# Kernel optimization log

Hardware: AMD Instinct MI355X
Metric: run time of the kernel (lower is better)

Reference implementation:

```python
import jax, jax.numpy as jnp
import numpy as np

B, S, E, H = 2, 2048, 1024, 16
D = E // H


def setup_inputs() -> dict:
    key = jax.random.key(0)
    ks = jax.random.split(key, 8)
    q = jax.random.normal(ks[0], (B, S, E), dtype=jnp.float32)
    k = jax.random.normal(ks[1], (B, S, E), dtype=jnp.float32)
    v = jax.random.normal(ks[2], (B, S, E), dtype=jnp.float32)
    mask = jax.random.randint(ks[3], (B, 1, 1, S), 0, 2, dtype=jnp.int32)
    sc = 1.0 / np.sqrt(E)
    W_qkv = jax.random.normal(ks[4], (3 * E, E), dtype=jnp.float32) * sc
    b_qkv = jnp.zeros((3 * E,), dtype=jnp.float32)
    W_out = jax.random.normal(ks[5], (E, E), dtype=jnp.float32) * sc
    b_out = jnp.zeros((E,), dtype=jnp.float32)
    return {"q": q, "k": k, "v": v, "mask": mask,
            "W_qkv": W_qkv, "b_qkv": b_qkv, "W_out": W_out, "b_out": b_out}


def reference(q, k, v, mask, W_qkv, b_qkv, W_out, b_out):
    # Fused qkv linear: q takes the Q-slice, k the K-slice, v the V-slice.
    qp = (q @ W_qkv[:E].T + b_qkv[:E]).reshape(B, S, H, D)
    kp = (k @ W_qkv[E:2 * E].T + b_qkv[E:2 * E]).reshape(B, S, H, D)
    vp = (v @ W_qkv[2 * E:].T + b_qkv[2 * E:]).reshape(B, S, H, D)
    # (B,H,S,S) scores -- NOTE: original module does NOT scale by sqrt(d)
    energy = jnp.einsum('nqhd,nkhd->nhqk', qp, kp)
    energy = jnp.where(mask == 0, jnp.float32(-1e20), energy)
    attention = jax.nn.softmax(energy, axis=-1)
    out = jnp.einsum('nhql,nlhd->nqhd', attention, vp).reshape(B, S, E)
    return out @ W_out.T + b_out
```

## Files before the change

kernel.cpp:

```cpp
#include <hip/hip_runtime.h>
#include <stdint.h>

constexpr int B_ = 2, S_ = 2048, E_ = 1024, H_ = 16, D_ = 64;
constexpr int M_ = B_ * S_;
constexpr size_t ME_ = (size_t)M_ * E_;

typedef unsigned short u16;
typedef __attribute__((ext_vector_type(8))) short short8;
typedef __attribute__((ext_vector_type(4))) float f32x4;

__device__ __forceinline__ float bf2f(u16 u) {
  union { uint32_t i; float f; } v; v.i = ((uint32_t)u) << 16; return v.f;
}
__device__ __forceinline__ u16 f2bf(float f) {
  uint32_t u = __float_as_uint(f);
  return (u16)((u + 0x7FFFu + ((u >> 16) & 1u)) >> 16);
}
__device__ __forceinline__ void tsplit(float x, u16& hi, u16& lo) {
  const uint32_t u = __float_as_uint(x);
  hi = (u16)(u >> 16);
  const float hif = __uint_as_float(u & 0xFFFF0000u);
  lo = (u16)(__float_as_uint(x - hif) >> 16);
}

__global__ __launch_bounds__(256) void split_f32_kernel(
    const float* __restrict__ src, u16* __restrict__ hi, u16* __restrict__ lo, int n4)
{
  const int i = blockIdx.x * 256 + threadIdx.x;
  if (i >= n4) return;
  const float4 x = ((const float4*)src)[i];
  ushort4 h, l;
  tsplit(x.x, h.x, l.x); tsplit(x.y, h.y, l.y);
  tsplit(x.z, h.z, l.z); tsplit(x.w, h.w, l.w);
  ((ushort4*)hi)[i] = h;
  ((ushort4*)lo)[i] = l;
}

__global__ __launch_bounds__(256) void mask_scan_kernel(
    const int* __restrict__ mask, int* __restrict__ cpos, int* __restrict__ nk)
{
  __shared__ int tmp[256];
  __shared__ int coff;
  const int b = blockIdx.x, t = threadIdx.x;
  if (t == 0) coff = 0;
  __syncthreads();
  for (int c = 0; c < S_; c += 256) {
    const int m = (mask[b * S_ + c + t] != 0) ? 1 : 0;
    int x = m;
    tmp[t] = x;
    __syncthreads();
#pragma unroll
    for (int off = 1; off < 256; off <<= 1) {
      const int v = (t >= off) ? tmp[t - off] : 0;
      __syncthreads();
      x += v;
      tmp[t] = x;
      __syncthreads();
    }
    const int base = coff;
    cpos[b * S_ + c + t] = base + x - m;
    __syncthreads();
    if (t == 255) coff = base + x;
    __syncthreads();
  }
  if (t == 0) nk[b] = coff;
}

__global__ __launch_bounds__(256) void gemm_qkv_kernel(
    const float* __restrict__ q, const float* __restrict__ k, const float* __restrict__ v,
    const u16* __restrict__ WHi, const u16* __restrict__ WLo,
    const float* __restrict__ bias,
    const int* __restrict__ Msk, const int* __restrict__ Cpos,
    u16* __restrict__ QpHi, u16* __restrict__ QpLo,
    u16* __restrict__ KpHi, u16* __restrict__ KpLo,
    u16* __restrict__ Vp)
{
  __shared__ __align__(16) short smem[15360];
  short* Ah = smem;
  short* Al = smem + 5120;
  short* Bh = smem + 10240;
  short* Bl = smem + 12800;

  const int t = threadIdx.x;
  const int m0 = blockIdx.x * 128;
  const int n0g = blockIdx.y * 64;
  const int proj = n0g >> 10;
  const int nloc = n0g & (E_ - 1);
  const float* A = (proj == 0) ? q : (proj == 1) ? k : v;
  const bool split = (proj < 2);

  const int w = t >> 6, lane = t & 63;
  const int g = lane >> 4, lc = lane & 15;
  const int wm = w & 1, wn = w >> 1;
  const int sra = t >> 1, sca = (t & 1) * 16;
  const int srb = t >> 2, scb = (t & 3) * 8;

  const float* Abp = A + (size_t)(m0 + sra) * E_ + sca;
  const u16* Bhb = WHi + (size_t)(n0g + srb) * E_ + scb;
  const u16* Blb = WLo + (size_t)(n0g + srb) * E_ + scb;

  f32x4 acc[4][2];
#pragma unroll
  for (int i = 0; i < 4; ++i)
#pragma unroll
    for (int j = 0; j < 2; ++j) acc[i][j] = (f32x4){0.f, 0.f, 0.f, 0.f};

  float4 ar[4]; short8 br, cr;
#pragma unroll
  for (int i = 0; i < 4; ++i) ar[i] = *(const float4*)(Abp + 4 * i);
  br = *(const short8*)(Bhb);
  if (split) cr = *(const short8*)(Blb);

  for (int k0 = 0; k0 < E_; k0 += 32) {
    __syncthreads();
#pragma unroll
    for (int i = 0; i < 4; ++i) {
      ushort4 h, l;
      tsplit(ar[i].x, h.x, l.x); tsplit(ar[i].y, h.y, l.y);
      tsplit(ar[i].z, h.z, l.z); tsplit(ar[i].w, h.w, l.w);
      *(ushort4*)&Ah[sra * 40 + sca + 4 * i] = h;
      if (split) *(ushort4*)&Al[sra * 40 + sca + 4 * i] = l;
    }
    *(short8*)&Bh[srb * 40 + scb] = br;
    if (split) *(short8*)&Bl[srb * 40 + scb] = cr;
    __syncthreads();
    if (k0 + 32 < E_) {
#pragma unroll
      for (int i = 0; i < 4; ++i) ar[i] = *(const float4*)(Abp + k0 + 32 + 4 * i);
      br = *(const short8*)(Bhb + k0 + 32);
      if (split) cr = *(const short8*)(Blb + k0 + 32);
    }

    short8 ah[4], al[4], bh[2], bl[2];
#pragma unroll
    for (int mt = 0; mt < 4; ++mt) {
      const int ro = (wm * 64 + mt * 16 + lc) * 40 + g * 8;
      ah[mt] = *(const short8*)&Ah[ro];
      if (split) al[mt] = *(const short8*)&Al[ro];
    }
#pragma unroll
    for (int nt = 0; nt < 2; ++nt) {
      const int ro = (wn * 32 + nt * 16 + lc) * 40 + g * 8;
      bh[nt] = *(const short8*)&Bh[ro];
      if (split) bl[nt] = *(const short8*)&Bl[ro];
    }
#pragma unroll
    for (int mt = 0; mt < 4; ++mt)
#pragma unroll
      for (int nt = 0; nt < 2; ++nt) {
        f32x4 a = acc[mt][nt];
        a = __builtin_amdgcn_mfma_f32_16x16x32_bf16(ah[mt], bh[nt], a, 0, 0, 0);
        if (split) {
          a = __builtin_amdgcn_mfma_f32_16x16x32_bf16(ah[mt], bl[nt], a, 0, 0, 0);
          a = __builtin_amdgcn_mfma_f32_16x16x32_bf16(al[mt], bh[nt], a, 0, 0, 0);
        }
        acc[mt][nt] = a;
      }
  }

  float bs[2];
#pragma unroll
  for (int nt = 0; nt < 2; ++nt) bs[nt] = bias[n0g + wn * 32 + nt * 16 + lc];

  if (proj < 2) {
    u16* Hi = (proj == 0) ? QpHi : KpHi;
    u16* Lo = (proj == 0) ? QpLo : KpLo;
    const int head = nloc >> 6;
    short* T = smem + w * 2560;
    const int mrow = m0 + wm * 64 + lane;
    const int bb = mrow >> 11, s = mrow & (S_ - 1);
    bool ok = true;
    int srow_out = s;
    if (proj == 1) {
      ok = (Msk[bb * S_ + s] != 0);
      srow_out = Cpos[bb * S_ + s];
    }
    const size_t rowb = (((size_t)(bb * H_ + head)) * S_ + srow_out) * D_ + wn * 32;
#pragma unroll
    for (int pass = 0; pass < 2; ++pass) {
      __syncthreads();
#pragma unroll
      for (int nt = 0; nt < 2; ++nt)
#pragma unroll
        for (int mt = 0; mt < 4; ++mt)
#pragma unroll
          for (int r = 0; r < 4; ++r) {
            const float val = acc[mt][nt][r] + bs[nt];
            const uint32_t u = __float_as_uint(val);
            u16 x;
            if (pass == 0) x = (u16)(u >> 16);
            else {
              const float hif = __uint_as_float(u & 0xFFFF0000u);
              x = (u16)(__float_as_uint(val - hif) >> 16);
            }
            T[(mt * 16 + g * 4 + r) * 40 + nt * 16 + lc] = (short)x;
          }
      __syncthreads();
      u16* dst = (pass == 0) ? Hi : Lo;
      if (ok) {
#pragma unroll
        for (int j = 0; j < 4; ++j)
          *(short8*)&dst[rowb + 8 * j] = *(const short8*)&T[lane * 40 + 8 * j];
      }
    }
  } else {
#pragma unroll
    for (int mt = 0; mt < 4; ++mt) {
      const int mrow = m0 + wm * 64 + mt * 16 + g * 4;
      const int bb = mrow >> 11, sbase = mrow & (S_ - 1);
      const int4 mk = *(const int4*)&Msk[bb * S_ + sbase];
      const int4 cp = *(const int4*)&Cpos[bb * S_ + sbase];
      const int mkA[4] = {mk.x, mk.y, mk.z, mk.w};
      const int cpA[4] = {cp.x, cp.y, cp.z, cp.w};
#pragma unroll
      for (int nt = 0; nt < 2; ++nt) {
        const int nE = nloc + wn * 32 + nt * 16 + lc;
        const int h = nE >> 6, d = nE & 63;
        const size_t rb = (((size_t)(bb * H_ + h)) * D_ + d) * S_;
#pragma unroll
        for (int r = 0; r < 4; ++r) {
          if (mkA[r]) Vp[rb + cpA[r]] = f2bf(acc[mt][nt][r] + bs[nt]);
        }
      }
    }
  }
}

__global__ __launch_bounds__(256, 4) void attn_mfma_kernel(
    const u16* __restrict__ QpHi, const u16* __restrict__ QpLo,
    const u16* __restrict__ KpHi, const u16* __restrict__ KpLo,
    const u16* __restrict__ Vp,
    const int* __restrict__ nkArr,
    u16* __restrict__ AOHi)
{
  __shared__ __align__(16) short sm[18432];
  short* Khi = sm;
  short* Klo = sm + 4608;
  short* Vt  = sm + 9216;
  short* Pb  = sm + 13824;

  const int t = threadIdx.x;
  const int w = t >> 6, lane = t & 63;
  const int g = lane >> 4, lc = lane & 15;
  const int bh = blockIdx.y;
  const int b = bh >> 4, hh = bh & 15;
  const int q0 = blockIdx.x * 64;
  const size_t hb = (size_t)bh * S_ * D_;
  const u16* QgH = QpHi + hb;
  const u16* QgL = QpLo + hb;
  const u16* KgH = KpHi + hb;
  const u16* KgL = KpLo + hb;
  const u16* Vg  = Vp + hb;
  short* Pw = Pb + w * 1152;

  const int nk = nkArr[b];
  const int kend = ((nk + 63) >> 6) << 6;

  short8 qh[2], ql[2];
  {
    const size_t base = (size_t)(q0 + 16 * w + lc) * D_ + 8 * g;
    qh[0] = *(const short8*)&QgH[base];
    qh[1] = *(const short8*)&QgH[base + 32];
    ql[0] = *(const short8*)&QgL[base];
    ql[1] = *(const short8*)&QgL[base + 32];
  }

  short8 ones8 = {0, 0, 0, 0, 0, 0, 0, 0};
  if (lc == 0) {
    const short o = (short)0x3F80;
    ones8 = (short8){o, o, o, o, o, o, o, o};
  }

  f32x4 O[4];
  f32x4 Ol = (f32x4){0.f, 0.f, 0.f, 0.f};
#pragma unroll
  for (int dt = 0; dt < 4; ++dt) O[dt] = (f32x4){0.f, 0.f, 0.f, 0.f};
  float mst[4] = {-INFINITY, -INFINITY, -INFINITY, -INFINITY};

  const int srow = t >> 2, sc16 = (t & 3) * 16;

  short8 kr[2], lr[2], vr[2];
  kr[0] = *(const short8*)&KgH[srow * D_ + sc16];
  kr[1] = *(const short8*)&KgH[srow * D_ + sc16 + 8];
  lr[0] = *(const short8*)&KgL[srow * D_ + sc16];
  lr[1] = *(const short8*)&KgL[srow * D_ + sc16 + 8];
  vr[0] = *(const short8*)&Vg[srow * S_ + sc16];
  vr[1] = *(const short8*)&Vg[srow * S_ + sc16 + 8];

  for (int kt = 0; kt < kend; kt += 64) {
    __syncthreads();
    *(short8*)&Khi[srow * 72 + sc16]     = kr[0];
    *(short8*)&Khi[srow * 72 + sc16 + 8] = kr[1];
    *(short8*)&Klo[srow * 72 + sc16]     = lr[0];
    *(short8*)&Klo[srow * 72 + sc16 + 8] = lr[1];
    *(short8*)&Vt[srow * 72 + sc16]      = vr[0];
    *(short8*)&Vt[srow * 72 + sc16 + 8]  = vr[1];
    __syncthreads();
    if (kt + 64 < kend) {
      const int kn = kt + 64;
      kr[0] = *(const short8*)&KgH[(kn + srow) * D_ + sc16];
      kr[1] = *(const short8*)&KgH[(kn + srow) * D_ + sc16 + 8];
      lr[0] = *(const short8*)&KgL[(kn + srow) * D_ + sc16];
      lr[1] = *(const short8*)&KgL[(kn + srow) * D_ + sc16 + 8];
      vr[0] = *(const short8*)&Vg[srow * S_ + kn + sc16];
      vr[1] = *(const short8*)&Vg[srow * S_ + kn + sc16 + 8];
    }

    f32x4 sc[4];
#pragma unroll
    for (int kt16 = 0; kt16 < 4; ++kt16) {
      const int ko = (16 * kt16 + lc) * 72 + 8 * g;
      const short8 kh0 = *(const short8*)&Khi[ko];
      const short8 kh1 = *(const short8*)&Khi[ko + 32];
      const short8 kl0 = *(const short8*)&Klo[ko];
      const short8 kl1 = *(const short8*)&Klo[ko + 32];
      f32x4 a = {0.f, 0.f, 0.f, 0.f};
      a = __builtin_amdgcn_mfma_f32_16x16x32_bf16(qh[0], kh0, a, 0, 0, 0);
      a = __builtin_amdgcn_mfma_f32_16x16x32_bf16(qh[1], kh1, a, 0, 0, 0);
      a = __builtin_amdgcn_mfma_f32_16x16x32_bf16(qh[0], kl0, a, 0, 0, 0);
      a = __builtin_amdgcn_mfma_f32_16x16x32_bf16(qh[1], kl1, a, 0, 0, 0);
      a = __builtin_amdgcn_mfma_f32_16x16x32_bf16(ql[0], kh0, a, 0, 0, 0);
      a = __builtin_amdgcn_mfma_f32_16x16x32_bf16(ql[1], kh1, a, 0, 0, 0);
      sc[kt16] = a;
    }

    if (kt + 64 > nk) {
#pragma unroll
      for (int kt16 = 0; kt16 < 4; ++kt16) {
        if (kt + 16 * kt16 + lc >= nk) {
          sc[kt16][0] = -1e20f; sc[kt16][1] = -1e20f;
          sc[kt16][2] = -1e20f; sc[kt16][3] = -1e20f;
        }
      }
    }

    float al[4];
#pragma unroll
    for (int r = 0; r < 4; ++r) {
      float vv = fmaxf(fmaxf(sc[0][r], sc[1][r]), fmaxf(sc[2][r], sc[3][r]));
      vv = fmaxf(vv, __shfl_xor(vv, 1));
      vv = fmaxf(vv, __shfl_xor(vv, 2));
      vv = fmaxf(vv, __shfl_xor(vv, 4));
      vv = fmaxf(vv, __shfl_xor(vv, 8));
      const float mn = fmaxf(mst[r], vv);
      al[r] = __expf(mst[r] - mn);
      mst[r] = mn;
    }
#pragma unroll
    for (int kt16 = 0; kt16 < 4; ++kt16) {
#pragma unroll
      for (int r = 0; r < 4; ++r)
        sc[kt16][r] = __expf(sc[kt16][r] - mst[r]);
    }
    const f32x4 alv = {al[0], al[1], al[2], al[3]};
    O[0] *= alv; O[1] *= alv; O[2] *= alv; O[3] *= alv;
    Ol *= alv;
#pragma unroll
    for (int kt16 = 0; kt16 < 4; ++kt16) {
#pragma unroll
      for (int r = 0; r < 4; ++r)
        Pw[(4 * g + r) * 72 + 16 * kt16 + lc] = (short)f2bf(sc[kt16][r]);
    }

    short8 pa[2];
    pa[0] = *(const short8*)&Pw[lc * 72 + 8 * g];
    pa[1] = *(const short8*)&Pw[lc * 72 + 32 + 8 * g];
    Ol = __builtin_amdgcn_mfma_f32_16x16x32_bf16(pa[0], ones8, Ol, 0, 0, 0);
    Ol = __builtin_amdgcn_mfma_f32_16x16x32_bf16(pa[1], ones8, Ol, 0, 0, 0);
#pragma unroll
    for (int dt = 0; dt < 4; ++dt) {
      const int vo = (16 * dt + lc) * 72 + 8 * g;
      const short8 vb0 = *(const short8*)&Vt[vo];
      const short8 vb1 = *(const short8*)&Vt[vo + 32];
      O[dt] = __builtin_amdgcn_mfma_f32_16x16x32_bf16(pa[0], vb0, O[dt], 0, 0, 0);
      O[dt] = __builtin_amdgcn_mfma_f32_16x16x32_bf16(pa[1], vb1, O[dt], 0, 0, 0);
    }
  }

#pragma unroll
  for (int r = 0; r < 4; ++r) {
    const float lv = __shfl(Ol[r], lane & 48);
    const float lir = 1.0f / lv;
    const int qrow = q0 + 16 * w + 4 * g + r;
    const size_t rowb = (size_t)(b * S_ + qrow) * E_ + hh * 64;
#pragma unroll
    for (int dt = 0; dt < 4; ++dt)
      AOHi[rowb + dt * 16 + lc] = f2bf(O[dt][r] * lir);
  }
}

__global__ __launch_bounds__(256) void gemm_out_kernel(
    const u16* __restrict__ AHi,
    const u16* __restrict__ WHi,
    const float* __restrict__ bias, float* __restrict__ out)
{
  __shared__ __align__(16) short Ah[128 * 40];
  __shared__ __align__(16) short Bh[128 * 40];

  const int t = threadIdx.x;
  const int m0 = blockIdx.x * 128;
  const int n0 = blockIdx.y * 128;
  const int w = t >> 6, lane = t & 63;
  const int g = lane >> 4, lc = lane & 15;
  const int wm = w & 1, wn = w >> 1;
  const int srow = t >> 1, sh = (t & 1) * 16;

  const u16* Ahb = AHi + (size_t)(m0 + srow) * E_ + sh;
  const u16* Bhb = WHi + (size_t)(n0 + srow) * E_ + sh;

  f32x4 acc[4][4];
#pragma unroll
  for (int i = 0; i < 4; ++i)
#pragma unroll
    for (int j = 0; j < 4; ++j) acc[i][j] = (f32x4){0.f, 0.f, 0.f, 0.f};

  short8 arr[2], brr[2];
  arr[0] = *(const short8*)(Ahb); arr[1] = *(const short8*)(Ahb + 8);
  brr[0] = *(const short8*)(Bhb); brr[1] = *(const short8*)(Bhb + 8);

  for (int k0 = 0; k0 < E_; k0 += 32) {
    __syncthreads();
    *(short8*)&Ah[srow * 40 + sh]     = arr[0];
    *(short8*)&Ah[srow * 40 + sh + 8] = arr[1];
    *(short8*)&Bh[srow * 40 + sh]     = brr[0];
    *(short8*)&Bh[srow * 40 + sh + 8] = brr[1];
    __syncthreads();
    if (k0 + 32 < E_) {
      arr[0] = *(const short8*)(Ahb + k0 + 32); arr[1] = *(const short8*)(Ahb + k0 + 40);
      brr[0] = *(const short8*)(Bhb + k0 + 32); brr[1] = *(const short8*)(Bhb + k0 + 40);
    }

    short8 ah[4], bh[4];
#pragma unroll
    for (int mt = 0; mt < 4; ++mt)
      ah[mt] = *(const short8*)&Ah[(wm * 64 + mt * 16 + lc) * 40 + g * 8];
#pragma unroll
    for (int nt = 0; nt < 4; ++nt)
      bh[nt] = *(const short8*)&Bh[(wn * 64 + nt * 16 + lc) * 40 + g * 8];
#pragma unroll
    for (int mt = 0; mt < 4; ++mt)
#pragma unroll
      for (int nt = 0; nt < 4; ++nt)
        acc[mt][nt] = __builtin_amdgcn_mfma_f32_16x16x32_bf16(ah[mt], bh[nt], acc[mt][nt], 0, 0, 0);
  }

  float bs[4];
#pragma unroll
  for (int nt = 0; nt < 4; ++nt) bs[nt] = bias[n0 + wn * 64 + nt * 16 + lc];
#pragma unroll
  for (int nt = 0; nt < 4; ++nt) {
    const int nc = n0 + wn * 64 + nt * 16 + lc;
#pragma unroll
    for (int mt = 0; mt < 4; ++mt) {
#pragma unroll
      for (int r = 0; r < 4; ++r) {
        const int mrow = m0 + wm * 64 + mt * 16 + g * 4 + r;
        out[(size_t)mrow * E_ + nc] = acc[mt][nt][r] + bs[nt];
      }
    }
  }
}

extern "C" void kernel_launch(void* const* d_in, const int* in_sizes, int n_in,
                              void* d_out, int out_size, void* d_ws, size_t ws_size,
                              hipStream_t stream) {
  const float* q    = (const float*)d_in[0];
  const float* k    = (const float*)d_in[1];
  const float* v    = (const float*)d_in[2];
  const int*   mask = (const int*)d_in[3];
  const float* Wqkv = (const float*)d_in[4];
  const float* bqkv = (const float*)d_in[5];
  const float* Wout = (const float*)d_in[6];
  const float* bout = (const float*)d_in[7];
  float* out = (float*)d_out;

  char* wsb = (char*)d_ws;
  u16* WqkvHi = (u16*)(wsb + 0);
  u16* WqkvLo = (u16*)(wsb + 6291456);
  u16* WoutHi = (u16*)(wsb + 12582912);
  int* Cpos   = (int*)(wsb + 14680064);
  int* Nk     = (int*)(wsb + 14680064 + 16384);
  u16* WoutLo = (u16*)(wsb + 14680064);
  u16* QpHi   = (u16*)(wsb + 16777216);
  u16* QpLo   = (u16*)(wsb + 25165824);
  u16* KpHi   = (u16*)(wsb + 33554432);
  u16* KpLo   = (u16*)(wsb + 41943040);
  u16* Vp     = (u16*)(wsb + 50331648);
  u16* AOHi   = (u16*)(wsb + 58720256);

  hipLaunchKernelGGL(split_f32_kernel, dim3(3072), dim3(256), 0, stream,
                     Wqkv, WqkvHi, WqkvLo, 786432);
  hipLaunchKernelGGL(split_f32_kernel, dim3(1024), dim3(256), 0, stream,
                     Wout, WoutHi, WoutLo, 262144);
  hipLaunchKernelGGL(mask_scan_kernel, dim3(B_), dim3(256), 0, stream,
                     mask, Cpos, Nk);
  hipMemsetAsync(Vp, 0, 8388608, stream);
  hipLaunchKernelGGL(gemm_qkv_kernel, dim3(M_ / 128, 48), dim3(256), 0, stream,
                     q, k, v, WqkvHi, WqkvLo, bqkv, mask, Cpos,
                     QpHi, QpLo, KpHi, KpLo, Vp);
  hipLaunchKernelGGL(attn_mfma_kernel, dim3(S_ / 64, B_ * H_), dim3(256), 0, stream,
                     QpHi, QpLo, KpHi, KpLo, Vp, Nk, AOHi);
  hipLaunchKernelGGL(gemm_out_kernel, dim3(M_ / 128, E_ / 128), dim3(256), 0, stream,
                     AOHi, WoutHi, bout, out);
}
```

Before: 294.4 us.

## Gather unmasked K/V rows before projection, double-buffer GEMM LDS, retile output GEMM

```diff
diff --git a/kernel.cpp b/kernel.cpp
--- a/kernel.cpp
+++ b/kernel.cpp
@@ -3,15 +3,11 @@
 
 constexpr int B_ = 2, S_ = 2048, E_ = 1024, H_ = 16, D_ = 64;
 constexpr int M_ = B_ * S_;
-constexpr size_t ME_ = (size_t)M_ * E_;
 
 typedef unsigned short u16;
 typedef __attribute__((ext_vector_type(8))) short short8;
 typedef __attribute__((ext_vector_type(4))) float f32x4;
 
-__device__ __forceinline__ float bf2f(u16 u) {
-  union { uint32_t i; float f; } v; v.i = ((uint32_t)u) << 16; return v.f;
-}
 __device__ __forceinline__ u16 f2bf(float f) {
   uint32_t u = __float_as_uint(f);
   return (u16)((u + 0x7FFFu + ((u >> 16) & 1u)) >> 16);
@@ -21,6 +17,13 @@
   hi = (u16)(u >> 16);
   const float hif = __uint_as_float(u & 0xFFFF0000u);
   lo = (u16)(__float_as_uint(x - hif) >> 16);
+}
+
+__device__ __forceinline__ void block_sync() {
+  asm volatile("" ::: "memory");
+  asm volatile("s_waitcnt lgkmcnt(0)" ::: "memory");
+  __builtin_amdgcn_s_barrier();
+  asm volatile("" ::: "memory");
 }
 
 __global__ __launch_bounds__(256) void split_f32_kernel(
@@ -37,11 +40,12 @@
 }
 
 __global__ __launch_bounds__(256) void mask_scan_kernel(
-    const int* __restrict__ mask, int* __restrict__ cpos, int* __restrict__ nk)
+    const int* __restrict__ mask, int* __restrict__ opos, int* __restrict__ nk)
 {
   __shared__ int tmp[256];
   __shared__ int coff;
   const int b = blockIdx.x, t = threadIdx.x;
+  for (int c = t; c < S_; c += 256) opos[b * S_ + c] = 0;
   if (t == 0) coff = 0;
   __syncthreads();
   for (int c = 0; c < S_; c += 256) {
@@ -58,7 +62,7 @@
       __syncthreads();
     }
     const int base = coff;
-    cpos[b * S_ + c + t] = base + x - m;
+    if (m) opos[b * S_ + base + x - 1] = c + t;
     __syncthreads();
     if (t == 255) coff = base + x;
     __syncthreads();
@@ -66,38 +70,45 @@
   if (t == 0) nk[b] = coff;
 }
 
-__global__ __launch_bounds__(256) void gemm_qkv_kernel(
+__global__ __launch_bounds__(256, 3) void gemm_qkv_kernel(
     const float* __restrict__ q, const float* __restrict__ k, const float* __restrict__ v,
     const u16* __restrict__ WHi, const u16* __restrict__ WLo,
     const float* __restrict__ bias,
-    const int* __restrict__ Msk, const int* __restrict__ Cpos,
+    const int* __restrict__ Opos, const int* __restrict__ NkArr,
     u16* __restrict__ QpHi, u16* __restrict__ QpLo,
     u16* __restrict__ KpHi, u16* __restrict__ KpLo,
     u16* __restrict__ Vp)
 {
-  __shared__ __align__(16) short smem[15360];
-  short* Ah = smem;
-  short* Al = smem + 5120;
-  short* Bh = smem + 10240;
-  short* Bl = smem + 12800;
+  __shared__ __align__(16) short smem[20480];
+  short* Ah0 = smem;
+  short* Al0 = smem + 5120;
+  short* Ah1 = smem + 10240;
+  short* Al1 = smem + 15360;
 
   const int t = threadIdx.x;
   const int m0 = blockIdx.x * 128;
   const int n0g = blockIdx.y * 64;
   const int proj = n0g >> 10;
   const int nloc = n0g & (E_ - 1);
+  const bool split = (proj < 2);
+  const int bb = m0 >> 11, mloc = m0 & (S_ - 1);
+  const int nkb = NkArr[bb];
+  if (proj != 0 && mloc >= nkb) return;
+
   const float* A = (proj == 0) ? q : (proj == 1) ? k : v;
-  const bool split = (proj < 2);
 
   const int w = t >> 6, lane = t & 63;
   const int g = lane >> 4, lc = lane & 15;
   const int wm = w & 1, wn = w >> 1;
   const int sra = t >> 1, sca = (t & 1) * 16;
-  const int srb = t >> 2, scb = (t & 3) * 8;
-
-  const float* Abp = A + (size_t)(m0 + sra) * E_ + sca;
-  const u16* Bhb = WHi + (size_t)(n0g + srb) * E_ + scb;
-  const u16* Blb = WLo + (size_t)(n0g + srb) * E_ + scb;
+
+  int arow;
+  if (proj == 0) arow = m0 + sra;
+  else arow = bb * S_ + (Opos[bb * S_ + mloc + sra] & (S_ - 1));
+  const float* Abp = A + (size_t)arow * E_ + sca;
+
+  const u16* BHrow = WHi + (size_t)(n0g + wn * 32 + lc) * E_ + 8 * g;
+  const u16* BLrow = WLo + (size_t)(n0g + wn * 32 + lc) * E_ + 8 * g;
 
   f32x4 acc[4][2];
 #pragma unroll
@@ -105,33 +116,29 @@
 #pragma unroll
     for (int j = 0; j < 2; ++j) acc[i][j] = (f32x4){0.f, 0.f, 0.f, 0.f};
 
-  float4 ar[4]; short8 br, cr;
-#pragma unroll
-  for (int i = 0; i < 4; ++i) ar[i] = *(const float4*)(Abp + 4 * i);
-  br = *(const short8*)(Bhb);
-  if (split) cr = *(const short8*)(Blb);
-
-  for (int k0 = 0; k0 < E_; k0 += 32) {
-    __syncthreads();
+  auto loadA = [&](float4* ar, int kk) {
+#pragma unroll
+    for (int i = 0; i < 4; ++i) ar[i] = *(const float4*)(Abp + kk + 4 * i);
+  };
+  auto writeA = [&](const float4* ar, short* Ah, short* Al) {
+    ushort hh[16], ll[16];
 #pragma unroll
     for (int i = 0; i < 4; ++i) {
-      ushort4 h, l;
-      tsplit(ar[i].x, h.x, l.x); tsplit(ar[i].y, h.y, l.y);
-      tsplit(ar[i].z, h.z, l.z); tsplit(ar[i].w, h.w, l.w);
-      *(ushort4*)&Ah[sra * 40 + sca + 4 * i] = h;
-      if (split) *(ushort4*)&Al[sra * 40 + sca + 4 * i] = l;
-    }
-    *(short8*)&Bh[srb * 40 + scb] = br;
-    if (split) *(short8*)&Bl[srb * 40 + scb] = cr;
-    __syncthreads();
-    if (k0 + 32 < E_) {
-#pragma unroll
-      for (int i = 0; i < 4; ++i) ar[i] = *(const float4*)(Abp + k0 + 32 + 4 * i);
-      br = *(const short8*)(Bhb + k0 + 32);
-      if (split) cr = *(const short8*)(Blb + k0 + 32);
-    }
-
-    short8 ah[4], al[4], bh[2], bl[2];
+      tsplit(ar[i].x, hh[4 * i + 0], ll[4 * i + 0]);
+      tsplit(ar[i].y, hh[4 * i + 1], ll[4 * i + 1]);
+      tsplit(ar[i].z, hh[4 * i + 2], ll[4 * i + 2]);
+      tsplit(ar[i].w, hh[4 * i + 3], ll[4 * i + 3]);
+    }
+    *(short8*)&Ah[sra * 40 + sca]     = *(const short8*)&hh[0];
+    *(short8*)&Ah[sra * 40 + sca + 8] = *(const short8*)&hh[8];
+    if (split) {
+      *(short8*)&Al[sra * 40 + sca]     = *(const short8*)&ll[0];
+      *(short8*)&Al[sra * 40 + sca + 8] = *(const short8*)&ll[8];
+    }
+  };
+  auto compute = [&](const short* Ah, const short* Al,
+                     short8 bh0, short8 bh1, short8 bl0, short8 bl1) {
+    short8 ah[4], al[4];
 #pragma unroll
     for (int mt = 0; mt < 4; ++mt) {
       const int ro = (wm * 64 + mt * 16 + lc) * 40 + g * 8;
@@ -139,23 +146,51 @@
       if (split) al[mt] = *(const short8*)&Al[ro];
     }
 #pragma unroll
-    for (int nt = 0; nt < 2; ++nt) {
-      const int ro = (wn * 32 + nt * 16 + lc) * 40 + g * 8;
-      bh[nt] = *(const short8*)&Bh[ro];
-      if (split) bl[nt] = *(const short8*)&Bl[ro];
-    }
-#pragma unroll
-    for (int mt = 0; mt < 4; ++mt)
-#pragma unroll
-      for (int nt = 0; nt < 2; ++nt) {
-        f32x4 a = acc[mt][nt];
-        a = __builtin_amdgcn_mfma_f32_16x16x32_bf16(ah[mt], bh[nt], a, 0, 0, 0);
-        if (split) {
-          a = __builtin_amdgcn_mfma_f32_16x16x32_bf16(ah[mt], bl[nt], a, 0, 0, 0);
-          a = __builtin_amdgcn_mfma_f32_16x16x32_bf16(al[mt], bh[nt], a, 0, 0, 0);
-        }
-        acc[mt][nt] = a;
+    for (int mt = 0; mt < 4; ++mt) {
+      f32x4 a0 = acc[mt][0], a1 = acc[mt][1];
+      a0 = __builtin_amdgcn_mfma_f32_16x16x32_bf16(ah[mt], bh0, a0, 0, 0, 0);
+      a1 = __builtin_amdgcn_mfma_f32_16x16x32_bf16(ah[mt], bh1, a1, 0, 0, 0);
+      if (split) {
+        a0 = __builtin_amdgcn_mfma_f32_16x16x32_bf16(ah[mt], bl0, a0, 0, 0, 0);
+        a0 = __builtin_amdgcn_mfma_f32_16x16x32_bf16(al[mt], bh0, a0, 0, 0, 0);
+        a1 = __builtin_amdgcn_mfma_f32_16x16x32_bf16(ah[mt], bl1, a1, 0, 0, 0);
+        a1 = __builtin_amdgcn_mfma_f32_16x16x32_bf16(al[mt], bh1, a1, 0, 0, 0);
       }
+      acc[mt][0] = a0; acc[mt][1] = a1;
+    }
+  };
+
+  float4 arA[4], arB[4];
+  short8 b0h0, b0h1, b1h0, b1h1;
+  short8 b0l0 = {}, b0l1 = {}, b1l0 = {}, b1l1 = {};
+  loadA(arA, 0);
+  b0h0 = *(const short8*)(BHrow);
+  b0h1 = *(const short8*)(BHrow + 16 * E_);
+  if (split) { b0l0 = *(const short8*)(BLrow); b0l1 = *(const short8*)(BLrow + 16 * E_); }
+
+  for (int k0 = 0; k0 < E_; k0 += 64) {
+    loadA(arB, k0 + 32);
+    writeA(arA, Ah0, Al0);
+    block_sync();
+    b1h0 = *(const short8*)(BHrow + k0 + 32);
+    b1h1 = *(const short8*)(BHrow + 16 * E_ + k0 + 32);
+    if (split) {
+      b1l0 = *(const short8*)(BLrow + k0 + 32);
+      b1l1 = *(const short8*)(BLrow + 16 * E_ + k0 + 32);
+    }
+    compute(Ah0, Al0, b0h0, b0h1, b0l0, b0l1);
+
+    const int kn = (k0 + 64 < E_) ? (k0 + 64) : 0;
+    loadA(arA, kn);
+    writeA(arB, Ah1, Al1);
+    block_sync();
+    b0h0 = *(const short8*)(BHrow + kn);
+    b0h1 = *(const short8*)(BHrow + 16 * E_ + kn);
+    if (split) {
+      b0l0 = *(const short8*)(BLrow + kn);
+      b0l1 = *(const short8*)(BLrow + 16 * E_ + kn);
+    }
+    compute(Ah1, Al1, b1h0, b1h1, b1l0, b1l1);
   }
 
   float bs[2];
@@ -167,15 +202,8 @@
     u16* Lo = (proj == 0) ? QpLo : KpLo;
     const int head = nloc >> 6;
     short* T = smem + w * 2560;
-    const int mrow = m0 + wm * 64 + lane;
-    const int bb = mrow >> 11, s = mrow & (S_ - 1);
-    bool ok = true;
-    int srow_out = s;
-    if (proj == 1) {
-      ok = (Msk[bb * S_ + s] != 0);
-      srow_out = Cpos[bb * S_ + s];
-    }
-    const size_t rowb = (((size_t)(bb * H_ + head)) * S_ + srow_out) * D_ + wn * 32;
+    const int s = (m0 + wm * 64 + lane) & (S_ - 1);
+    const size_t rowb = (((size_t)(bb * H_ + head)) * S_ + s) * D_ + wn * 32;
 #pragma unroll
     for (int pass = 0; pass < 2; ++pass) {
       __syncthreads();
@@ -197,21 +225,14 @@
           }
       __syncthreads();
       u16* dst = (pass == 0) ? Hi : Lo;
-      if (ok) {
-#pragma unroll
-        for (int j = 0; j < 4; ++j)
-          *(short8*)&dst[rowb + 8 * j] = *(const short8*)&T[lane * 40 + 8 * j];
-      }
+#pragma unroll
+      for (int j = 0; j < 4; ++j)
+        *(short8*)&dst[rowb + 8 * j] = *(const short8*)&T[lane * 40 + 8 * j];
     }
   } else {
 #pragma unroll
     for (int mt = 0; mt < 4; ++mt) {
-      const int mrow = m0 + wm * 64 + mt * 16 + g * 4;
-      const int bb = mrow >> 11, sbase = mrow & (S_ - 1);
-      const int4 mk = *(const int4*)&Msk[bb * S_ + sbase];
-      const int4 cp = *(const int4*)&Cpos[bb * S_ + sbase];
-      const int mkA[4] = {mk.x, mk.y, mk.z, mk.w};
-      const int cpA[4] = {cp.x, cp.y, cp.z, cp.w};
+      const int jb = mloc + wm * 64 + mt * 16 + g * 4;
 #pragma unroll
       for (int nt = 0; nt < 2; ++nt) {
         const int nE = nloc + wn * 32 + nt * 16 + lc;
@@ -219,7 +240,7 @@
         const size_t rb = (((size_t)(bb * H_ + h)) * D_ + d) * S_;
 #pragma unroll
         for (int r = 0; r < 4; ++r) {
-          if (mkA[r]) Vp[rb + cpA[r]] = f2bf(acc[mt][nt][r] + bs[nt]);
+          if (jb + r < nkb) Vp[rb + jb + r] = f2bf(acc[mt][nt][r] + bs[nt]);
         }
       }
     }
@@ -394,69 +415,66 @@
     const u16* __restrict__ WHi,
     const float* __restrict__ bias, float* __restrict__ out)
 {
-  __shared__ __align__(16) short Ah[128 * 40];
-  __shared__ __align__(16) short Bh[128 * 40];
+  __shared__ __align__(16) short smem[5120];
+  short* A0 = smem;
+  short* A1 = smem + 2560;
 
   const int t = threadIdx.x;
-  const int m0 = blockIdx.x * 128;
-  const int n0 = blockIdx.y * 128;
+  const int m0 = blockIdx.x * 64;
+  const int n0 = blockIdx.y * 64;
   const int w = t >> 6, lane = t & 63;
   const int g = lane >> 4, lc = lane & 15;
-  const int wm = w & 1, wn = w >> 1;
-  const int srow = t >> 1, sh = (t & 1) * 16;
-
-  const u16* Ahb = AHi + (size_t)(m0 + srow) * E_ + sh;
-  const u16* Bhb = WHi + (size_t)(n0 + srow) * E_ + sh;
-
-  f32x4 acc[4][4];
-#pragma unroll
-  for (int i = 0; i < 4; ++i)
-#pragma unroll
-    for (int j = 0; j < 4; ++j) acc[i][j] = (f32x4){0.f, 0.f, 0.f, 0.f};
-
-  short8 arr[2], brr[2];
-  arr[0] = *(const short8*)(Ahb); arr[1] = *(const short8*)(Ahb + 8);
-  brr[0] = *(const short8*)(Bhb); brr[1] = *(const short8*)(Bhb + 8);
-
-  for (int k0 = 0; k0 < E_; k0 += 32) {
-    __syncthreads();
-    *(short8*)&Ah[srow * 40 + sh]     = arr[0];
-    *(short8*)&Ah[srow * 40 + sh + 8] = arr[1];
-    *(short8*)&Bh[srow * 40 + sh]     = brr[0];
-    *(short8*)&Bh[srow * 40 + sh + 8] = brr[1];
-    __syncthreads();
-    if (k0 + 32 < E_) {
-      arr[0] = *(const short8*)(Ahb + k0 + 32); arr[1] = *(const short8*)(Ahb + k0 + 40);
-      brr[0] = *(const short8*)(Bhb + k0 + 32); brr[1] = *(const short8*)(Bhb + k0 + 40);
-    }
-
-    short8 ah[4], bh[4];
-#pragma unroll
-    for (int mt = 0; mt < 4; ++mt)
-      ah[mt] = *(const short8*)&Ah[(wm * 64 + mt * 16 + lc) * 40 + g * 8];
-#pragma unroll
-    for (int nt = 0; nt < 4; ++nt)
-      bh[nt] = *(const short8*)&Bh[(wn * 64 + nt * 16 + lc) * 40 + g * 8];
-#pragma unroll
-    for (int mt = 0; mt < 4; ++mt)
-#pragma unroll
-      for (int nt = 0; nt < 4; ++nt)
-        acc[mt][nt] = __builtin_amdgcn_mfma_f32_16x16x32_bf16(ah[mt], bh[nt], acc[mt][nt], 0, 0, 0);
-  }
-
-  float bs[4];
-#pragma unroll
-  for (int nt = 0; nt < 4; ++nt) bs[nt] = bias[n0 + wn * 64 + nt * 16 + lc];
-#pragma unroll
-  for (int nt = 0; nt < 4; ++nt) {
-    const int nc = n0 + wn * 64 + nt * 16 + lc;
-#pragma unroll
-    for (int mt = 0; mt < 4; ++mt) {
-#pragma unroll
-      for (int r = 0; r < 4; ++r) {
-        const int mrow = m0 + wm * 64 + mt * 16 + g * 4 + r;
-        out[(size_t)mrow * E_ + nc] = acc[mt][nt][r] + bs[nt];
-      }
+  const int srb = t >> 2, scb = (t & 3) * 8;
+
+  const u16* Abp = AHi + (size_t)(m0 + srb) * E_ + scb;
+  const u16* Brow = WHi + (size_t)(n0 + w * 16 + lc) * E_ + 8 * g;
+
+  f32x4 acc[4];
+#pragma unroll
+  for (int i = 0; i < 4; ++i) acc[i] = (f32x4){0.f, 0.f, 0.f, 0.f};
+
+  short8 aA, aB, b0, b1;
+  aA = *(const short8*)(Abp);
+  b0 = *(const short8*)(Brow);
+
+  for (int k0 = 0; k0 < E_; k0 += 64) {
+    aB = *(const short8*)(Abp + k0 + 32);
+    *(short8*)&A0[srb * 40 + scb] = aA;
+    block_sync();
+    b1 = *(const short8*)(Brow + k0 + 32);
+    {
+      short8 ah[4];
+#pragma unroll
+      for (int mt = 0; mt < 4; ++mt)
+        ah[mt] = *(const short8*)&A0[(mt * 16 + lc) * 40 + g * 8];
+#pragma unroll
+      for (int mt = 0; mt < 4; ++mt)
+        acc[mt] = __builtin_amdgcn_mfma_f32_16x16x32_bf16(ah[mt], b0, acc[mt], 0, 0, 0);
+    }
+    const int kn = (k0 + 64 < E_) ? (k0 + 64) : 0;
+    aA = *(const short8*)(Abp + kn);
+    *(short8*)&A1[srb * 40 + scb] = aB;
+    block_sync();
+    b0 = *(const short8*)(Brow + kn);
+    {
+      short8 ah[4];
+#pragma unroll
+      for (int mt = 0; mt < 4; ++mt)
+        ah[mt] = *(const short8*)&A1[(mt * 16 + lc) * 40 + g * 8];
+#pragma unroll
+      for (int mt = 0; mt < 4; ++mt)
+        acc[mt] = __builtin_amdgcn_mfma_f32_16x16x32_bf16(ah[mt], b1, acc[mt], 0, 0, 0);
+    }
+  }
+
+  const int nc = n0 + w * 16 + lc;
+  const float bsc = bias[nc];
+#pragma unroll
+  for (int mt = 0; mt < 4; ++mt) {
+#pragma unroll
+    for (int r = 0; r < 4; ++r) {
+      const int mrow = m0 + mt * 16 + g * 4 + r;
+      out[(size_t)mrow * E_ + nc] = acc[mt][r] + bsc;
     }
   }
 }
@@ -478,7 +496,7 @@
   u16* WqkvHi = (u16*)(wsb + 0);
   u16* WqkvLo = (u16*)(wsb + 6291456);
   u16* WoutHi = (u16*)(wsb + 12582912);
-  int* Cpos   = (int*)(wsb + 14680064);
+  int* Opos   = (int*)(wsb + 14680064);
   int* Nk     = (int*)(wsb + 14680064 + 16384);
   u16* WoutLo = (u16*)(wsb + 14680064);
   u16* QpHi   = (u16*)(wsb + 16777216);
@@ -493,13 +511,13 @@
   hipLaunchKernelGGL(split_f32_kernel, dim3(1024), dim3(256), 0, stream,
                      Wout, WoutHi, WoutLo, 262144);
   hipLaunchKernelGGL(mask_scan_kernel, dim3(B_), dim3(256), 0, stream,
-                     mask, Cpos, Nk);
+                     mask, Opos, Nk);
   hipMemsetAsync(Vp, 0, 8388608, stream);
   hipLaunchKernelGGL(gemm_qkv_kernel, dim3(M_ / 128, 48), dim3(256), 0, stream,
-                     q, k, v, WqkvHi, WqkvLo, bqkv, mask, Cpos,
+                     q, k, v, WqkvHi, WqkvLo, bqkv, Opos, Nk,
                      QpHi, QpLo, KpHi, KpLo, Vp);
   hipLaunchKernelGGL(attn_mfma_kernel, dim3(S_ / 64, B_ * H_), dim3(256), 0, stream,
                      QpHi, QpLo, KpHi, KpLo, Vp, Nk, AOHi);
-  hipLaunchKernelGGL(gemm_out_kernel, dim3(M_ / 128, E_ / 128), dim3(256), 0, stream,
+  hipLaunchKernelGGL(gemm_out_kernel, dim3(M_ / 64, E_ / 64), dim3(256), 0, stream,
                      AOHi, WoutHi, bout, out);
 }
```

Result: slower. 331.5 us (+12.6%).

## Gather unmasked key rows before K/V projection and shrink output GEMM tiles

Applied to the files above, without the earlier changes.

```diff
diff --git a/kernel.cpp b/kernel.cpp
--- a/kernel.cpp
+++ b/kernel.cpp
@@ -3,15 +3,11 @@
 
 constexpr int B_ = 2, S_ = 2048, E_ = 1024, H_ = 16, D_ = 64;
 constexpr int M_ = B_ * S_;
-constexpr size_t ME_ = (size_t)M_ * E_;
 
 typedef unsigned short u16;
 typedef __attribute__((ext_vector_type(8))) short short8;
 typedef __attribute__((ext_vector_type(4))) float f32x4;
 
-__device__ __forceinline__ float bf2f(u16 u) {
-  union { uint32_t i; float f; } v; v.i = ((uint32_t)u) << 16; return v.f;
-}
 __device__ __forceinline__ u16 f2bf(float f) {
   uint32_t u = __float_as_uint(f);
   return (u16)((u + 0x7FFFu + ((u >> 16) & 1u)) >> 16);
@@ -37,11 +33,12 @@
 }
 
 __global__ __launch_bounds__(256) void mask_scan_kernel(
-    const int* __restrict__ mask, int* __restrict__ cpos, int* __restrict__ nk)
+    const int* __restrict__ mask, int* __restrict__ opos, int* __restrict__ nk)
 {
   __shared__ int tmp[256];
   __shared__ int coff;
   const int b = blockIdx.x, t = threadIdx.x;
+  for (int c = t; c < S_; c += 256) opos[b * S_ + c] = 0;
   if (t == 0) coff = 0;
   __syncthreads();
   for (int c = 0; c < S_; c += 256) {
@@ -58,7 +55,7 @@
       __syncthreads();
     }
     const int base = coff;
-    cpos[b * S_ + c + t] = base + x - m;
+    if (m) opos[b * S_ + base + x - 1] = c + t;
     __syncthreads();
     if (t == 255) coff = base + x;
     __syncthreads();
@@ -70,7 +67,7 @@
     const float* __restrict__ q, const float* __restrict__ k, const float* __restrict__ v,
     const u16* __restrict__ WHi, const u16* __restrict__ WLo,
     const float* __restrict__ bias,
-    const int* __restrict__ Msk, const int* __restrict__ Cpos,
+    const int* __restrict__ Opos, const int* __restrict__ NkArr,
     u16* __restrict__ QpHi, u16* __restrict__ QpLo,
     u16* __restrict__ KpHi, u16* __restrict__ KpLo,
     u16* __restrict__ Vp)
@@ -86,8 +83,12 @@
   const int n0g = blockIdx.y * 64;
   const int proj = n0g >> 10;
   const int nloc = n0g & (E_ - 1);
+  const bool split = (proj < 2);
+  const int bb = m0 >> 11, mloc = m0 & (S_ - 1);
+  const int nkb = NkArr[bb];
+  if (proj != 0 && mloc >= nkb) return;
+
   const float* A = (proj == 0) ? q : (proj == 1) ? k : v;
-  const bool split = (proj < 2);
 
   const int w = t >> 6, lane = t & 63;
   const int g = lane >> 4, lc = lane & 15;
@@ -95,7 +96,10 @@
   const int sra = t >> 1, sca = (t & 1) * 16;
   const int srb = t >> 2, scb = (t & 3) * 8;
 
-  const float* Abp = A + (size_t)(m0 + sra) * E_ + sca;
+  int arow;
+  if (proj == 0) arow = m0 + sra;
+  else arow = bb * S_ + (Opos[bb * S_ + mloc + sra] & (S_ - 1));
+  const float* Abp = A + (size_t)arow * E_ + sca;
   const u16* Bhb = WHi + (size_t)(n0g + srb) * E_ + scb;
   const u16* Blb = WLo + (size_t)(n0g + srb) * E_ + scb;
 
@@ -167,15 +171,8 @@
     u16* Lo = (proj == 0) ? QpLo : KpLo;
     const int head = nloc >> 6;
     short* T = smem + w * 2560;
-    const int mrow = m0 + wm * 64 + lane;
-    const int bb = mrow >> 11, s = mrow & (S_ - 1);
-    bool ok = true;
-    int srow_out = s;
-    if (proj == 1) {
-      ok = (Msk[bb * S_ + s] != 0);
-      srow_out = Cpos[bb * S_ + s];
-    }
-    const size_t rowb = (((size_t)(bb * H_ + head)) * S_ + srow_out) * D_ + wn * 32;
+    const int s = (m0 + wm * 64 + lane) & (S_ - 1);
+    const size_t rowb = (((size_t)(bb * H_ + head)) * S_ + s) * D_ + wn * 32;
 #pragma unroll
     for (int pass = 0; pass < 2; ++pass) {
       __syncthreads();
@@ -197,21 +194,14 @@
           }
       __syncthreads();
       u16* dst = (pass == 0) ? Hi : Lo;
-      if (ok) {
-#pragma unroll
-        for (int j = 0; j < 4; ++j)
-          *(short8*)&dst[rowb + 8 * j] = *(const short8*)&T[lane * 40 + 8 * j];
-      }
+#pragma unroll
+      for (int j = 0; j < 4; ++j)
+        *(short8*)&dst[rowb + 8 * j] = *(const short8*)&T[lane * 40 + 8 * j];
     }
   } else {
 #pragma unroll
     for (int mt = 0; mt < 4; ++mt) {
-      const int mrow = m0 + wm * 64 + mt * 16 + g * 4;
-      const int bb = mrow >> 11, sbase = mrow & (S_ - 1);
-      const int4 mk = *(const int4*)&Msk[bb * S_ + sbase];
-      const int4 cp = *(const int4*)&Cpos[bb * S_ + sbase];
-      const int mkA[4] = {mk.x, mk.y, mk.z, mk.w};
-      const int cpA[4] = {cp.x, cp.y, cp.z, cp.w};
+      const int jb = mloc + wm * 64 + mt * 16 + g * 4;
 #pragma unroll
       for (int nt = 0; nt < 2; ++nt) {
         const int nE = nloc + wn * 32 + nt * 16 + lc;
@@ -219,7 +209,7 @@
         const size_t rb = (((size_t)(bb * H_ + h)) * D_ + d) * S_;
 #pragma unroll
         for (int r = 0; r < 4; ++r) {
-          if (mkA[r]) Vp[rb + cpA[r]] = f2bf(acc[mt][nt][r] + bs[nt]);
+          if (jb + r < nkb) Vp[rb + jb + r] = f2bf(acc[mt][nt][r] + bs[nt]);
         }
       }
     }
@@ -394,67 +384,66 @@
     const u16* __restrict__ WHi,
     const float* __restrict__ bias, float* __restrict__ out)
 {
-  __shared__ __align__(16) short Ah[128 * 40];
-  __shared__ __align__(16) short Bh[128 * 40];
+  __shared__ __align__(16) short smem[5120];
+  short* Ah = smem;
+  short* Bh = smem + 2560;
 
   const int t = threadIdx.x;
-  const int m0 = blockIdx.x * 128;
-  const int n0 = blockIdx.y * 128;
+  const int m0 = blockIdx.x * 64;
+  const int n0 = blockIdx.y * 64;
   const int w = t >> 6, lane = t & 63;
   const int g = lane >> 4, lc = lane & 15;
   const int wm = w & 1, wn = w >> 1;
-  const int srow = t >> 1, sh = (t & 1) * 16;
-
-  const u16* Ahb = AHi + (size_t)(m0 + srow) * E_ + sh;
-  const u16* Bhb = WHi + (size_t)(n0 + srow) * E_ + sh;
-
-  f32x4 acc[4][4];
-#pragma unroll
-  for (int i = 0; i < 4; ++i)
-#pragma unroll
-    for (int j = 0; j < 4; ++j) acc[i][j] = (f32x4){0.f, 0.f, 0.f, 0.f};
-
-  short8 arr[2], brr[2];
-  arr[0] = *(const short8*)(Ahb); arr[1] = *(const short8*)(Ahb + 8);
-  brr[0] = *(const short8*)(Bhb); brr[1] = *(const short8*)(Bhb + 8);
+  const int sr = t >> 2, sc = (t & 3) * 8;
+
+  const u16* Ahb = AHi + (size_t)(m0 + sr) * E_ + sc;
+  const u16* Bhb = WHi + (size_t)(n0 + sr) * E_ + sc;
+
+  f32x4 acc[2][2];
+#pragma unroll
+  for (int i = 0; i < 2; ++i)
+#pragma unroll
+    for (int j = 0; j < 2; ++j) acc[i][j] = (f32x4){0.f, 0.f, 0.f, 0.f};
+
+  short8 arr, brr;
+  arr = *(const short8*)(Ahb);
+  brr = *(const short8*)(Bhb);
 
   for (int k0 = 0; k0 < E_; k0 += 32) {
     __syncthreads();
-    *(short8*)&Ah[srow * 40 + sh]     = arr[0];
-    *(short8*)&Ah[srow * 40 + sh + 8] = arr[1];
-    *(short8*)&Bh[srow * 40 + sh]     = brr[0];
-    *(short8*)&Bh[srow * 40 + sh + 8] = brr[1];
+    *(short8*)&Ah[sr * 40 + sc] = arr;
+    *(short8*)&Bh[sr * 40 + sc] = brr;
     __syncthreads();
     if (k0 + 32 < E_) {
-      arr[0] = *(const short8*)(Ahb + k0 + 32); arr[1] = *(const short8*)(Ahb + k0 + 40);
-      brr[0] = *(const short8*)(Bhb + k0 + 32); brr[1] = *(const short8*)(Bhb + k0 + 40);
-    }
-
-    short8 ah[4], bh[4];
-#pragma unroll
-    for (int mt = 0; mt < 4; ++mt)
-      ah[mt] = *(const short8*)&Ah[(wm * 64 + mt * 16 + lc) * 40 + g * 8];
-#pragma unroll
-    for (int nt = 0; nt < 4; ++nt)
-      bh[nt] = *(const short8*)&Bh[(wn * 64 + nt * 16 + lc) * 40 + g * 8];
-#pragma unroll
-    for (int mt = 0; mt < 4; ++mt)
-#pragma unroll
-      for (int nt = 0; nt < 4; ++nt)
+      arr = *(const short8*)(Ahb + k0 + 32);
+      brr = *(const short8*)(Bhb + k0 + 32);
+    }
+
+    short8 ah[2], bh[2];
+#pragma unroll
+    for (int mt = 0; mt < 2; ++mt)
+      ah[mt] = *(const short8*)&Ah[(wm * 32 + mt * 16 + lc) * 40 + g * 8];
+#pragma unroll
+    for (int nt = 0; nt < 2; ++nt)
+      bh[nt] = *(const short8*)&Bh[(wn * 32 + nt * 16 + lc) * 40 + g * 8];
+#pragma unroll
+    for (int mt = 0; mt < 2; ++mt)
+#pragma unroll
+      for (int nt = 0; nt < 2; ++nt)
         acc[mt][nt] = __builtin_amdgcn_mfma_f32_16x16x32_bf16(ah[mt], bh[nt], acc[mt][nt], 0, 0, 0);
   }
 
-  float bs[4];
-#pragma unroll
-  for (int nt = 0; nt < 4; ++nt) bs[nt] = bias[n0 + wn * 64 + nt * 16 + lc];
-#pragma unroll
-  for (int nt = 0; nt < 4; ++nt) {
-    const int nc = n0 + wn * 64 + nt * 16 + lc;
-#pragma unroll
-    for (int mt = 0; mt < 4; ++mt) {
+  float bs[2];
+#pragma unroll
+  for (int nt = 0; nt < 2; ++nt) bs[nt] = bias[n0 + wn * 32 + nt * 16 + lc];
+#pragma unroll
+  for (int nt = 0; nt < 2; ++nt) {
+    const int nc = n0 + wn * 32 + nt * 16 + lc;
+#pragma unroll
+    for (int mt = 0; mt < 2; ++mt) {
 #pragma unroll
       for (int r = 0; r < 4; ++r) {
-        const int mrow = m0 + wm * 64 + mt * 16 + g * 4 + r;
+        const int mrow = m0 + wm * 32 + mt * 16 + g * 4 + r;
         out[(size_t)mrow * E_ + nc] = acc[mt][nt][r] + bs[nt];
       }
     }
@@ -478,7 +467,7 @@
   u16* WqkvHi = (u16*)(wsb + 0);
   u16* WqkvLo = (u16*)(wsb + 6291456);
   u16* WoutHi = (u16*)(wsb + 12582912);
-  int* Cpos   = (int*)(wsb + 14680064);
+  int* Opos   = (int*)(wsb + 14680064);
   int* Nk     = (int*)(wsb + 14680064 + 16384);
   u16* WoutLo = (u16*)(wsb + 14680064);
   u16* QpHi   = (u16*)(wsb + 16777216);
@@ -493,13 +482,13 @@
   hipLaunchKernelGGL(split_f32_kernel, dim3(1024), dim3(256), 0, stream,
                      Wout, WoutHi, WoutLo, 262144);
   hipLaunchKernelGGL(mask_scan_kernel, dim3(B_), dim3(256), 0, stream,
-                     mask, Cpos, Nk);
+                     mask, Opos, Nk);
   hipMemsetAsync(Vp, 0, 8388608, stream);
   hipLaunchKernelGGL(gemm_qkv_kernel, dim3(M_ / 128, 48), dim3(256), 0, stream,
-                     q, k, v, WqkvHi, WqkvLo, bqkv, mask, Cpos,
+                     q, k, v, WqkvHi, WqkvLo, bqkv, Opos, Nk,
                      QpHi, QpLo, KpHi, KpLo, Vp);
   hipLaunchKernelGGL(attn_mfma_kernel, dim3(S_ / 64, B_ * H_), dim3(256), 0, stream,
                      QpHi, QpLo, KpHi, KpLo, Vp, Nk, AOHi);
-  hipLaunchKernelGGL(gemm_out_kernel, dim3(M_ / 128, E_ / 128), dim3(256), 0, stream,
+  hipLaunchKernelGGL(gemm_out_kernel, dim3(M_ / 64, E_ / 64), dim3(256), 0, stream,
                      AOHi, WoutHi, bout, out);
 }
```

Result: no change. 296.9 us (+0.9%).
